# Kernel optimization log

Measured on AMD Instinct MI355X. Metric: run time of the kernel, lower is better.

## Reference

```python
import jax, jax.numpy as jnp
import numpy as np

B, L, E = 2, 2048, 1024
H, DKV = 16, 64


def setup_inputs() -> dict:
    key = jax.random.key(0)
    k1, k2 = jax.random.split(key)
    X = jax.random.normal(k1, (B, L, E), dtype=jnp.float32)
    # nn.Linear(embed_dim, n_heads*3*d_kv): weight stored here as [in, out]
    W_qkv = jax.random.normal(k2, (E, 3 * H * DKV), dtype=jnp.float32) * (1.0 / np.sqrt(E))
    b_qkv = jnp.zeros((3 * H * DKV,), dtype=jnp.float32)
    return {"X": X, "W_qkv": W_qkv, "b_qkv": b_qkv}


def reference(X, W_qkv, b_qkv):
    b, l, _ = X.shape
    # fused QKV projection, then 'b l (h 3*dkv)' -> [b, l, h, 3*dkv] -> chunk(3)
    qkv = (X @ W_qkv + b_qkv).reshape(b, l, H, 3 * DKV)
    Q, K, V = jnp.split(qkv, 3, axis=-1)  # each [b, l, h, dkv]
    # attn_scores: einsum('bkhd, blhd -> bhkl') / sqrt(d_kv)
    scores = jnp.einsum('bkhd,blhd->bhkl', Q, K) / np.sqrt(DKV).astype(np.float32)
    # attn_mask defaults to None -> no causal masking applied
    attn_weights = jax.nn.softmax(scores, axis=-1)  # [b, h, l, l]
    return attn_weights
```

## Files before the change

### kernel.cpp

```cpp
#include <hip/hip_runtime.h>
#include <hip/hip_bf16.h>

typedef _Float16 half4v __attribute__((ext_vector_type(4)));
typedef _Float16 half8v __attribute__((ext_vector_type(8)));
typedef float float4v __attribute__((ext_vector_type(4)));

#define L_SEQ 2048
#define EMB 1024
#define NH 16
#define DKV 64

__device__ inline void gll16(const void* g, void* l) {
  __builtin_amdgcn_global_load_lds((const __attribute__((address_space(1))) void*)g,
                                   (__attribute__((address_space(3))) void*)l, 16, 0, 0);
}

__global__ __launch_bounds__(256) void xcast_kernel(const float* __restrict__ X,
                                                    _Float16* __restrict__ X16) {
  size_t i = ((size_t)blockIdx.x * 256 + threadIdx.x) * 8;
  float4v v0 = *(const float4v*)(X + i);
  float4v v1 = *(const float4v*)(X + i + 4);
  half8v h;
  h[0] = (_Float16)v0[0]; h[1] = (_Float16)v0[1]; h[2] = (_Float16)v0[2]; h[3] = (_Float16)v0[3];
  h[4] = (_Float16)v1[0]; h[5] = (_Float16)v1[1]; h[6] = (_Float16)v1[2]; h[7] = (_Float16)v1[3];
  *(half8v*)(X16 + i) = h;
}

__global__ __launch_bounds__(256) void wpack_kernel(const float* __restrict__ W,
                                                    _Float16* __restrict__ Wt) {
  __shared__ float tile[32][33];
  int n0 = blockIdx.x * 32;
  int k0 = blockIdx.y * 32;
  int h = n0 >> 7;
  int wc = h * 192 + (n0 & 127);
  int tx = threadIdx.x & 31;
  int ty = threadIdx.x >> 5;
#pragma unroll
  for (int i = 0; i < 4; ++i) {
    int k = ty + i * 8;
    tile[k][tx] = W[(size_t)(k0 + k) * 3072 + wc + tx];
  }
  __syncthreads();
#pragma unroll
  for (int i = 0; i < 4; ++i) {
    int n = ty + i * 8;
    Wt[(size_t)(n0 + n) * 1024 + k0 + tx] = (_Float16)tile[tx][n];
  }
}

__global__ __launch_bounds__(256) void qk_gemm_kernel(const _Float16* __restrict__ X16,
                                                      const _Float16* __restrict__ Wt,
                                                      const float* __restrict__ bias,
                                                      _Float16* __restrict__ Qh,
                                                      _Float16* __restrict__ Kh) {
  __shared__ _Float16 As[128 * 32];
  __shared__ _Float16 Bs[128 * 32];
  int n0 = blockIdx.x * 128;
  int m0 = blockIdx.y * 128;
  int t = threadIdx.x;
  int l = t & 63;
  int wv = t >> 6;
  int wm = wv >> 1, wn = wv & 1;
  int cl = l & 15, ko = (l >> 4) * 8;
  int srow = (l >> 2);
  int scol = (l & 3) * 8;
  float4v acc[4][4] = {};
  for (int k0 = 0; k0 < 1024; k0 += 32) {
#pragma unroll
    for (int c = 0; c < 2; ++c) {
      int rbase = wv * 32 + c * 16;
      gll16(X16 + (size_t)(m0 + rbase + srow) * 1024 + k0 + scol, &As[rbase * 32]);
      gll16(Wt + (size_t)(n0 + rbase + srow) * 1024 + k0 + scol, &Bs[rbase * 32]);
    }
    __syncthreads();
    half8v a[4], b[4];
#pragma unroll
    for (int mt = 0; mt < 4; ++mt) a[mt] = *(const half8v*)(&As[(wm * 64 + mt * 16 + cl) * 32 + ko]);
#pragma unroll
    for (int nt = 0; nt < 4; ++nt) b[nt] = *(const half8v*)(&Bs[(wn * 64 + nt * 16 + cl) * 32 + ko]);
#pragma unroll
    for (int mt = 0; mt < 4; ++mt)
#pragma unroll
      for (int nt = 0; nt < 4; ++nt)
        acc[mt][nt] = __builtin_amdgcn_mfma_f32_16x16x32_f16(a[mt], b[nt], acc[mt][nt], 0, 0, 0);
    __syncthreads();
  }
#pragma unroll
  for (int mt = 0; mt < 4; ++mt) {
#pragma unroll
    for (int nt = 0; nt < 4; ++nt) {
      int n_g = n0 + wn * 64 + nt * 16 + cl;
      int hh = n_g >> 7, rr = n_g & 127;
      float bv = bias[hh * 192 + rr];
      _Float16* dstbase = (rr < 64) ? Qh : Kh;
      int d = rr & 63;
#pragma unroll
      for (int r = 0; r < 4; ++r) {
        int row_g = m0 + wm * 64 + mt * 16 + (l >> 4) * 4 + r;
        int bb = row_g >> 11, lr = row_g & 2047;
        dstbase[(((size_t)bb * NH + hh) * L_SEQ + lr) * DKV + d] = (_Float16)(acc[mt][nt][r] + bv);
      }
    }
  }
}

__global__ __launch_bounds__(256) void attn_softmax_kernel(const _Float16* __restrict__ Qh,
                                                           const _Float16* __restrict__ Kh,
                                                           float* __restrict__ out) {
  __shared__ _Float16 Ks[2][64 * 64];
  __shared__ float Ps[4][16 * 64];
  int id = blockIdx.x;
  int xcd = id & 7;
  int rest = id >> 3;
  int rb = rest & 31;
  int bh = ((rest >> 5) << 3) + xcd;
  int t = threadIdx.x;
  int l = t & 63;
  int wv = t >> 6;
  int cl = l & 15;
  int hi = l >> 4;
  int qbase = rb * 64 + wv * 16;
  const _Float16* Qb = Qh + ((size_t)bh * L_SEQ + qbase) * DKV;
  const _Float16* Kb = Kh + (size_t)bh * L_SEQ * DKV;
  half8v aq0 = *(const half8v*)(Qb + cl * DKV + hi * 8);
  half8v aq1 = *(const half8v*)(Qb + cl * DKV + 32 + hi * 8);
  const float SC = 0.18033688011112042f;

#define STAGE(bufi, j0)                                                     \
  {                                                                         \
    _Pragma("unroll") for (int c = 0; c < 2; ++c) {                         \
      int gi = (wv * 2 + c) * 64 + l;                                       \
      int r_ = gi >> 3, s_ = gi & 7;                                        \
      gll16(Kb + (size_t)((j0) + r_) * DKV + 8 * (s_ ^ (r_ & 7)),           \
            &Ks[bufi][(wv * 2 + c) * 512]);                                 \
    }                                                                       \
  }

  float lsum = 0.f;
  int buf = 0;
  STAGE(0, 0);
  __syncthreads();
  for (int jt = 0; jt < 32; ++jt) {
    if (jt + 1 < 32) STAGE(buf ^ 1, (jt + 1) * 64);
#pragma unroll
    for (int s4 = 0; s4 < 4; ++s4) {
      int row = s4 * 16 + cl;
      half8v b0 = *(const half8v*)(&Ks[buf][row * 64 + 8 * (hi ^ (cl & 7))]);
      half8v b1 = *(const half8v*)(&Ks[buf][row * 64 + 8 * ((hi + 4) ^ (cl & 7))]);
      float4v acc = {};
      acc = __builtin_amdgcn_mfma_f32_16x16x32_f16(b0, aq0, acc, 0, 0, 0);
      acc = __builtin_amdgcn_mfma_f32_16x16x32_f16(b1, aq1, acc, 0, 0, 0);
      lsum += __builtin_amdgcn_exp2f(acc[0] * SC) + __builtin_amdgcn_exp2f(acc[1] * SC) +
              __builtin_amdgcn_exp2f(acc[2] * SC) + __builtin_amdgcn_exp2f(acc[3] * SC);
    }
    __syncthreads();
    buf ^= 1;
  }
  lsum += __shfl_xor(lsum, 16);
  lsum += __shfl_xor(lsum, 32);
  float inv = 1.0f / lsum;

  float* Pw = Ps[wv];
  size_t orow = (size_t)bh * L_SEQ + qbase;
  buf = 0;
  STAGE(0, 0);
  __syncthreads();
  for (int jt = 0; jt < 32; ++jt) {
    if (jt + 1 < 32) STAGE(buf ^ 1, (jt + 1) * 64);
#pragma unroll
    for (int s4 = 0; s4 < 4; ++s4) {
      int row = s4 * 16 + cl;
      half8v b0 = *(const half8v*)(&Ks[buf][row * 64 + 8 * (hi ^ (cl & 7))]);
      half8v b1 = *(const half8v*)(&Ks[buf][row * 64 + 8 * ((hi + 4) ^ (cl & 7))]);
      float4v acc = {};
      acc = __builtin_amdgcn_mfma_f32_16x16x32_f16(b0, aq0, acc, 0, 0, 0);
      acc = __builtin_amdgcn_mfma_f32_16x16x32_f16(b1, aq1, acc, 0, 0, 0);
      float4v pv;
      pv[0] = __builtin_amdgcn_exp2f(acc[0] * SC) * inv;
      pv[1] = __builtin_amdgcn_exp2f(acc[1] * SC) * inv;
      pv[2] = __builtin_amdgcn_exp2f(acc[2] * SC) * inv;
      pv[3] = __builtin_amdgcn_exp2f(acc[3] * SC) * inv;
      int jj = s4 * 4 + hi;
      *(float4v*)(&Pw[cl * 64 + 4 * (jj ^ cl)]) = pv;
    }
#pragma unroll
    for (int i = 0; i < 4; ++i) {
      int row = i * 4 + hi;
      int g = cl;
      float4v v = *(const float4v*)(&Pw[row * 64 + 4 * (g ^ row)]);
      *(float4v*)(out + (orow + row) * L_SEQ + jt * 64 + 4 * g) = v;
    }
    __syncthreads();
    buf ^= 1;
  }
#undef STAGE
}

extern "C" void kernel_launch(void* const* d_in, const int* in_sizes, int n_in,
                              void* d_out, int out_size, void* d_ws, size_t ws_size,
                              hipStream_t stream) {
  const float* X = (const float*)d_in[0];
  const float* W = (const float*)d_in[1];
  const float* bias = (const float*)d_in[2];
  float* out = (float*)d_out;
  char* ws = (char*)d_ws;
  _Float16* Wt = (_Float16*)ws;
  _Float16* Qh = (_Float16*)(ws + (4ull << 20));
  _Float16* Kh = (_Float16*)(ws + (12ull << 20));
  _Float16* X16 = (_Float16*)(ws + (20ull << 20));

  xcast_kernel<<<2048, 256, 0, stream>>>(X, X16);
  wpack_kernel<<<dim3(64, 32), 256, 0, stream>>>(W, Wt);
  qk_gemm_kernel<<<dim3(16, 32), 256, 0, stream>>>(X16, Wt, bias, Qh, Kh);
  attn_softmax_kernel<<<1024, 256, 0, stream>>>(Qh, Kh, out);
}
```

Baseline: 193.9 us.

## Use 32x32 MFMA tiles with 128-row K stages and direct nontemporal output stores

Restructures the attention-softmax kernel so each wave computes 32x32 score tiles with the 32x32x16 MFMA, splitting query rows and key columns across waves. K tiles are staged in 128-row chunks. Row sums are combined through shared memory and folded into the exponent as a log2 offset, which removes the per-element multiply. The LDS transpose of probabilities is dropped in favour of direct nontemporal scalar stores. Those stores give 128-byte contiguous runs per row instead of the earlier float4 vector stores, which could reduce write efficiency. The change also adds a 4-block occupancy hint.

```diff
diff --git a/kernel.cpp b/kernel.cpp
--- a/kernel.cpp
+++ b/kernel.cpp
@@ -4,6 +4,7 @@
 typedef _Float16 half4v __attribute__((ext_vector_type(4)));
 typedef _Float16 half8v __attribute__((ext_vector_type(8)));
 typedef float float4v __attribute__((ext_vector_type(4)));
+typedef float float16v __attribute__((ext_vector_type(16)));
 
 #define L_SEQ 2048
 #define EMB 1024
@@ -104,11 +105,11 @@
   }
 }
 
-__global__ __launch_bounds__(256) void attn_softmax_kernel(const _Float16* __restrict__ Qh,
-                                                           const _Float16* __restrict__ Kh,
-                                                           float* __restrict__ out) {
-  __shared__ _Float16 Ks[2][64 * 64];
-  __shared__ float Ps[4][16 * 64];
+__global__ __launch_bounds__(256, 4) void attn_softmax_kernel(const _Float16* __restrict__ Qh,
+                                                              const _Float16* __restrict__ Kh,
+                                                              float* __restrict__ out) {
+  __shared__ _Float16 Ks[2][128 * 64];
+  __shared__ float sums[4][32];
   int id = blockIdx.x;
   int xcd = id & 7;
   int rest = id >> 3;
@@ -117,22 +118,27 @@
   int t = threadIdx.x;
   int l = t & 63;
   int wv = t >> 6;
-  int cl = l & 15;
-  int hi = l >> 4;
-  int qbase = rb * 64 + wv * 16;
+  int lj = l & 31;
+  int hk = l >> 5;
+  int qh = wv & 1;
+  int jh = wv >> 1;
+  int qbase = rb * 64;
   const _Float16* Qb = Qh + ((size_t)bh * L_SEQ + qbase) * DKV;
   const _Float16* Kb = Kh + (size_t)bh * L_SEQ * DKV;
-  half8v aq0 = *(const half8v*)(Qb + cl * DKV + hi * 8);
-  half8v aq1 = *(const half8v*)(Qb + cl * DKV + 32 + hi * 8);
   const float SC = 0.18033688011112042f;
+
+  half8v bq[4];
+#pragma unroll
+  for (int ks = 0; ks < 4; ++ks)
+    bq[ks] = *(const half8v*)(Qb + (size_t)(qh * 32 + lj) * DKV + ks * 16 + hk * 8);
 
 #define STAGE(bufi, j0)                                                     \
   {                                                                         \
-    _Pragma("unroll") for (int c = 0; c < 2; ++c) {                         \
-      int gi = (wv * 2 + c) * 64 + l;                                       \
+    _Pragma("unroll") for (int c = 0; c < 4; ++c) {                         \
+      int gi = (wv * 4 + c) * 64 + l;                                       \
       int r_ = gi >> 3, s_ = gi & 7;                                        \
       gll16(Kb + (size_t)((j0) + r_) * DKV + 8 * (s_ ^ (r_ & 7)),           \
-            &Ks[bufi][(wv * 2 + c) * 512]);                                 \
+            &Ks[bufi][(wv * 4 + c) * 512]);                                 \
     }                                                                       \
   }
 
@@ -140,55 +146,62 @@
   int buf = 0;
   STAGE(0, 0);
   __syncthreads();
-  for (int jt = 0; jt < 32; ++jt) {
-    if (jt + 1 < 32) STAGE(buf ^ 1, (jt + 1) * 64);
-#pragma unroll
-    for (int s4 = 0; s4 < 4; ++s4) {
-      int row = s4 * 16 + cl;
-      half8v b0 = *(const half8v*)(&Ks[buf][row * 64 + 8 * (hi ^ (cl & 7))]);
-      half8v b1 = *(const half8v*)(&Ks[buf][row * 64 + 8 * ((hi + 4) ^ (cl & 7))]);
-      float4v acc = {};
-      acc = __builtin_amdgcn_mfma_f32_16x16x32_f16(b0, aq0, acc, 0, 0, 0);
-      acc = __builtin_amdgcn_mfma_f32_16x16x32_f16(b1, aq1, acc, 0, 0, 0);
-      lsum += __builtin_amdgcn_exp2f(acc[0] * SC) + __builtin_amdgcn_exp2f(acc[1] * SC) +
-              __builtin_amdgcn_exp2f(acc[2] * SC) + __builtin_amdgcn_exp2f(acc[3] * SC);
+  for (int s = 0; s < 16; ++s) {
+    if (s + 1 < 16) STAGE(buf ^ 1, (s + 1) * 128);
+#pragma unroll
+    for (int q2 = 0; q2 < 2; ++q2) {
+      int jq = jh * 2 + q2;
+      int krow = jq * 32 + lj;
+      half8v bk[4];
+#pragma unroll
+      for (int ks = 0; ks < 4; ++ks)
+        bk[ks] = *(const half8v*)(&Ks[buf][krow * 64 + 8 * ((2 * ks + hk) ^ (krow & 7))]);
+      float16v acc = {};
+#pragma unroll
+      for (int ks = 0; ks < 4; ++ks)
+        acc = __builtin_amdgcn_mfma_f32_32x32x16_f16(bk[ks], bq[ks], acc, 0, 0, 0);
+#pragma unroll
+      for (int i = 0; i < 16; ++i) lsum += __builtin_amdgcn_exp2f(acc[i] * SC);
     }
     __syncthreads();
     buf ^= 1;
   }
-  lsum += __shfl_xor(lsum, 16);
   lsum += __shfl_xor(lsum, 32);
-  float inv = 1.0f / lsum;
-
-  float* Pw = Ps[wv];
-  size_t orow = (size_t)bh * L_SEQ + qbase;
+  if (l < 32) sums[wv][lj] = lsum;
+  __syncthreads();
+
+  float cc[16];
+#pragma unroll
+  for (int i = 0; i < 16; ++i) {
+    int qo = (i & 3) + 8 * (i >> 2) + 4 * hk;
+    cc[i] = -__log2f(sums[qh][qo] + sums[qh + 2][qo]);
+  }
+
+  size_t orow0 = ((size_t)bh * L_SEQ + qbase + qh * 32) * L_SEQ;
+  STAGE(0, 0);
+  __syncthreads();
   buf = 0;
-  STAGE(0, 0);
-  __syncthreads();
-  for (int jt = 0; jt < 32; ++jt) {
-    if (jt + 1 < 32) STAGE(buf ^ 1, (jt + 1) * 64);
-#pragma unroll
-    for (int s4 = 0; s4 < 4; ++s4) {
-      int row = s4 * 16 + cl;
-      half8v b0 = *(const half8v*)(&Ks[buf][row * 64 + 8 * (hi ^ (cl & 7))]);
-      half8v b1 = *(const half8v*)(&Ks[buf][row * 64 + 8 * ((hi + 4) ^ (cl & 7))]);
-      float4v acc = {};
-      acc = __builtin_amdgcn_mfma_f32_16x16x32_f16(b0, aq0, acc, 0, 0, 0);
-      acc = __builtin_amdgcn_mfma_f32_16x16x32_f16(b1, aq1, acc, 0, 0, 0);
-      float4v pv;
-      pv[0] = __builtin_amdgcn_exp2f(acc[0] * SC) * inv;
-      pv[1] = __builtin_amdgcn_exp2f(acc[1] * SC) * inv;
-      pv[2] = __builtin_amdgcn_exp2f(acc[2] * SC) * inv;
-      pv[3] = __builtin_amdgcn_exp2f(acc[3] * SC) * inv;
-      int jj = s4 * 4 + hi;
-      *(float4v*)(&Pw[cl * 64 + 4 * (jj ^ cl)]) = pv;
-    }
-#pragma unroll
-    for (int i = 0; i < 4; ++i) {
-      int row = i * 4 + hi;
-      int g = cl;
-      float4v v = *(const float4v*)(&Pw[row * 64 + 4 * (g ^ row)]);
-      *(float4v*)(out + (orow + row) * L_SEQ + jt * 64 + 4 * g) = v;
+  for (int s = 0; s < 16; ++s) {
+    if (s + 1 < 16) STAGE(buf ^ 1, (s + 1) * 128);
+#pragma unroll
+    for (int q2 = 0; q2 < 2; ++q2) {
+      int jq = jh * 2 + q2;
+      int krow = jq * 32 + lj;
+      half8v bk[4];
+#pragma unroll
+      for (int ks = 0; ks < 4; ++ks)
+        bk[ks] = *(const half8v*)(&Ks[buf][krow * 64 + 8 * ((2 * ks + hk) ^ (krow & 7))]);
+      float16v acc = {};
+#pragma unroll
+      for (int ks = 0; ks < 4; ++ks)
+        acc = __builtin_amdgcn_mfma_f32_32x32x16_f16(bq[ks], bk[ks], acc, 0, 0, 0);
+      size_t col = (size_t)s * 128 + jq * 32 + lj;
+#pragma unroll
+      for (int i = 0; i < 16; ++i) {
+        float p = __builtin_amdgcn_exp2f(acc[i] * SC + cc[i]);
+        int qo = (i & 3) + 8 * (i >> 2) + 4 * hk;
+        __builtin_nontemporal_store(p, out + orow0 + (size_t)qo * L_SEQ + col);
+      }
     }
     __syncthreads();
     buf ^= 1;
```

Result: faster. 162.8 us (-16.1%).
